# Kernel tuning notes

Measured on AMD Instinct MI355X. Metric: run time of the kernel, lower is better.

The kernel has to match this reference:

```python
import jax, jax.numpy as jnp
import numpy as np

H = 128       # hidden size
IN = 6        # input size
OUT = 1       # output size
B, T = 128, 2048


def setup_inputs() -> dict:
    key = jax.random.key(0)
    ks = jax.random.split(key, 16)
    s = 1.0 / np.sqrt(H)  # PyTorch LSTM init: U(-1/sqrt(H), 1/sqrt(H))
    u = lambda k, shape: jax.random.uniform(k, shape, jnp.float32, -s, s)
    inp = {"x": jax.random.normal(ks[0], (B, T, IN), jnp.float32)}
    in_sizes = [IN, H, H]
    for l in range(3):
        inp[f"W_ih{l}"] = u(ks[1 + 4 * l], (4 * H, in_sizes[l]))
        inp[f"W_hh{l}"] = u(ks[2 + 4 * l], (4 * H, H))
        inp[f"b_ih{l}"] = u(ks[3 + 4 * l], (4 * H,))
        inp[f"b_hh{l}"] = u(ks[4 + 4 * l], (4 * H,))
    inp["W_out"] = u(ks[13], (OUT, H))
    inp["b_out"] = u(ks[14], (OUT,))
    return inp


def _lstm_layer(x, W_ih, W_hh, b):
    # x: [B, T, D_in]; precompute input contribution once, scan the recurrence.
    xg = jnp.einsum("bti,gi->btg", x, W_ih) + b  # [B, T, 4H]
    h0 = jnp.zeros((x.shape[0], H), x.dtype)
    c0 = jnp.zeros((x.shape[0], H), x.dtype)

    def step(carry, xg_t):
        h, c = carry
        g = xg_t + h @ W_hh.T                     # [B, 4H]
        i, f, gg, o = jnp.split(g, 4, axis=-1)    # PyTorch gate order i,f,g,o
        i = jax.nn.sigmoid(i)
        f = jax.nn.sigmoid(f)
        gg = jnp.tanh(gg)
        o = jax.nn.sigmoid(o)
        c = f * c + i * gg
        h = o * jnp.tanh(c)
        return (h, c), h

    _, hs = jax.lax.scan(step, (h0, c0), jnp.swapaxes(xg, 0, 1))  # hs: [T, B, H]
    return jnp.swapaxes(hs, 0, 1)


def reference(x, W_ih0, W_hh0, b_ih0, b_hh0, W_ih1, W_hh1, b_ih1, b_hh1,
              W_ih2, W_hh2, b_ih2, b_hh2, W_out, b_out):
    # 3-layer LSTM (dropout inactive in eval mode) + linear head on last step.
    h = _lstm_layer(x, W_ih0, W_hh0, b_ih0 + b_hh0)
    h = _lstm_layer(h, W_ih1, W_hh1, b_ih1 + b_hh1)
    h = _lstm_layer(h, W_ih2, W_hh2, b_ih2 + b_hh2)
    return h[:, -1, :] @ W_out.T + b_out  # [B, 1]
```

## Files before the change

### kernel.cpp

```cpp
#include <hip/hip_runtime.h>

#define B_ 128
#define T_ 2048
#define H_ 128
#define IN_ 6
#define GRP_ 8
#define NGRP_ (T_ / GRP_)
#define CHUNK_ 32
#define NCHUNK_ (T_ / CHUNK_)
#define FLAG_STRIDE_ 64
#define HS_ 144
#define XGRING_ 3
#define XGSLOT_ (CHUNK_ * 8192)
#define NFLAGS_ 272

typedef _Float16 f16x8 __attribute__((ext_vector_type(8)));
typedef float    f32x4 __attribute__((ext_vector_type(4)));

__device__ __forceinline__ unsigned short f2h_u(float f) {
  union { _Float16 h; unsigned short u; } v; v.h = (_Float16)f; return v.u;
}
__device__ __forceinline__ unsigned int pack2(float a, float b) {
  return (unsigned int)f2h_u(a) | ((unsigned int)f2h_u(b) << 16);
}
__device__ __forceinline__ float sigf_(float x) {
  return __builtin_amdgcn_rcpf(1.0f + __expf(-x));
}
__device__ __forceinline__ float tanhf_(float x) {
  return 2.0f * __builtin_amdgcn_rcpf(1.0f + __expf(-2.0f * x)) - 1.0f;
}
__device__ __forceinline__ f16x8 load_w8(const float* __restrict__ p) {
  f16x8 r;
#pragma unroll
  for (int i = 0; i < 8; ++i) r[i] = (_Float16)p[i];
  return r;
}

__global__ void init_flags(unsigned int* flags) {
  flags[blockIdx.x * 256 + threadIdx.x] = 0u;
}

#define BARRIER_LGKM()                                              \
  do {                                                              \
    asm volatile("s_waitcnt lgkmcnt(0)" ::: "memory");              \
    __builtin_amdgcn_s_barrier();                                   \
    __builtin_amdgcn_sched_barrier(0);                              \
  } while (0)

#define PUBLISH_FENCE()                                             \
  do {                                                              \
    asm volatile("s_waitcnt vmcnt(0)" ::: "memory");                \
    __builtin_amdgcn_s_barrier();                                   \
  } while (0)

#define MFMA16(A, B, C) __builtin_amdgcn_mfma_f32_16x16x32_f16((A), (B), (C), 0, 0, 0)

__global__ __launch_bounds__(512, 2)
void lstm_pipe(const float* __restrict__ x,
               const float* __restrict__ Wih0, const float* __restrict__ Whh0,
               const float* __restrict__ bih0, const float* __restrict__ bhh0,
               const float* __restrict__ Wih1, const float* __restrict__ Whh1,
               const float* __restrict__ bih1, const float* __restrict__ bhh1,
               const float* __restrict__ Wih2, const float* __restrict__ Whh2,
               const float* __restrict__ bih2, const float* __restrict__ bhh2,
               unsigned short* __restrict__ region,
               float* __restrict__ xg,
               unsigned int* __restrict__ state_h,
               unsigned int* __restrict__ flags)
{
  const int bid  = blockIdx.x;
  const int tid  = threadIdx.x;
  const int lane = tid & 63;
  const int wv   = tid >> 6;
  const int n16  = lane & 15;
  const int quad = lane >> 4;

  __shared__ unsigned short smem[32 * 16 * HS_];
  __shared__ int s_have;

#define WAITP(ptr_, need_, have_)                                   \
  do {                                                              \
    if ((have_) < (need_)) {                                        \
      if (tid == 0) {                                               \
        int v = (int)__hip_atomic_load(ptr_, __ATOMIC_RELAXED,      \
                                       __HIP_MEMORY_SCOPE_AGENT);   \
        while (v < (need_)) {                                       \
          __builtin_amdgcn_s_sleep(2);                              \
          v = (int)__hip_atomic_load(ptr_, __ATOMIC_RELAXED,        \
                                     __HIP_MEMORY_SCOPE_AGENT);     \
        }                                                           \
        (void)__hip_atomic_load(ptr_, __ATOMIC_ACQUIRE,             \
                                __HIP_MEMORY_SCOPE_AGENT);          \
        s_have = v;                                                 \
      }                                                             \
      __syncthreads();                                              \
      (have_) = s_have;                                             \
    }                                                               \
  } while (0)

  if (bid >= 96) {
    const int gi = bid - 96;
    const int gl = 1 + (gi >> 3);
    const int bg = gi & 7;
    const int b8 = n16 & 7;
    const float* Wih = (gl == 1) ? Wih1 : Wih2;
    const float* bih = (gl == 1) ? bih1 : bih2;
    const float* bhh = (gl == 1) ? bhh1 : bhh2;
    float* xgo = xg + (size_t)((gl - 1) * 8 + bg) * (XGRING_ * (size_t)XGSLOT_);
    unsigned int* fhp[4]; unsigned int* fcp[4];
#pragma unroll
    for (int q = 0; q < 4; ++q) {
      fhp[q] = &flags[((gl - 1) * 32 + 4 * bg + q) * FLAG_STRIDE_];
      fcp[q] = &flags[(144 + (gl - 1) * 64 + 4 * bg + q) * FLAG_STRIDE_];
    }
    unsigned int* fx_out = &flags[(128 + (gl - 1) * 8 + bg) * FLAG_STRIDE_];

    f16x8 wih[4][4];
#pragma unroll
    for (int j = 0; j < 4; ++j)
#pragma unroll
      for (int kc = 0; kc < 4; ++kc)
        wih[j][kc] = load_w8(Wih + (size_t)(j * 128 + 16 * wv + n16) * H_ + kc * 32 + quad * 8);
    f32x4 bias4[4];
#pragma unroll
    for (int j = 0; j < 4; ++j)
#pragma unroll
      for (int r = 0; r < 4; ++r) {
        int row = j * 128 + 16 * wv + quad * 4 + r;
        bias4[j][r] = bih[row] + bhh[row];
      }

    int haveh0 = 0, haveh1 = 0, haveh2 = 0, haveh3 = 0;
    int havec0 = 0, havec1 = 0, havec2 = 0, havec3 = 0;
    const int tt = tid >> 4, bb = tid & 15;
    const int swk = bb & 7;
    for (int k = 0; k < NCHUNK_; ++k) {
      WAITP(fhp[0], k + 1, haveh0);
      WAITP(fhp[1], k + 1, haveh1);
      WAITP(fhp[2], k + 1, haveh2);
      WAITP(fhp[3], k + 1, haveh3);
      if (k >= XGRING_) {
        WAITP(fcp[0], k - (XGRING_ - 1), havec0);
        WAITP(fcp[1], k - (XGRING_ - 1), havec1);
        WAITP(fcp[2], k - (XGRING_ - 1), havec2);
        WAITP(fcp[3], k - (XGRING_ - 1), havec3);
      }
      {
        const uint4* gp = (const uint4*)(region +
            ((size_t)(bg * 16 + bb) * T_ + (size_t)(CHUNK_ * k + tt)) * H_);
        uint4* lp = (uint4*)&smem[(tt * 16 + bb) * HS_];
#pragma unroll
        for (int i = 0; i < 16; ++i) lp[i ^ swk] = gp[i];
      }
      __syncthreads();
      const int slot = k % XGRING_;
      for (int t = 0; t < CHUNK_; ++t) {
        f16x8 hi4[4];
#pragma unroll
        for (int kc = 0; kc < 4; ++kc)
          hi4[kc] = *(const f16x8*)&smem[(t * 16 + n16) * HS_ +
                                         ((kc * 32 + quad * 8) ^ (b8 << 3))];
        float* xp = xgo + (size_t)(slot * CHUNK_ + t) * 8192 + quad * 64 + n16 * 4;
#pragma unroll
        for (int j = 0; j < 4; ++j) {
          f32x4 a = bias4[j];
#pragma unroll
          for (int kc = 0; kc < 4; ++kc)
            a = MFMA16(wih[j][kc], hi4[kc], a);
          *(f32x4*)(xp + (size_t)(8 * j + wv) * 256) = a;
        }
      }
      __syncthreads();
      if (tid == 0)
        __hip_atomic_store(fx_out, (unsigned int)(k + 1),
                           __ATOMIC_RELEASE, __HIP_MEMORY_SCOPE_AGENT);
    }
    return;
  }

  const int layer = bid >> 5;
  const int sl    = bid & 31;
  const int bcol  = n16 & 3;
  const int rr    = n16 >> 2;
  const int batch = sl * 4 + bcol;
  const float* Whh = (layer == 0) ? Whh0 : ((layer == 1) ? Whh1 : Whh2);

  unsigned short* hstate = smem;
  unsigned short* xb = smem + 2 * 4 * HS_;

  f16x8 whh[4][4];
#pragma unroll
  for (int j = 0; j < 4; ++j)
#pragma unroll
    for (int kc = 0; kc < 4; ++kc)
      whh[j][kc] = load_w8(Whh + (size_t)(j * 128 + 16 * wv + n16) * H_ + kc * 32 + quad * 8);

  for (int i = tid; i < (2 * 4 * HS_) / 2; i += 512) ((unsigned int*)smem)[i] = 0u;

  float cc_ = 0.f;
  unsigned short dh16[GRP_];
  const bool r2 = (rr & 2) != 0, r1 = (rr & 1) != 0;
  const int hcol = 16 * wv + 4 * quad + rr;
  const int wswz = (((hcol >> 3) ^ bcol) << 3) | (hcol & 7);
  unsigned int* fh_out = (layer < 2) ? &flags[(layer * 32 + sl) * FLAG_STRIDE_] : nullptr;

#define SEL3(a_) (r1 ? (r2 ? (a_)[3] : (a_)[1]) : (r2 ? (a_)[2] : (a_)[0]))

  if (layer == 0) {
    f32x4 bias4[4];
#pragma unroll
    for (int j = 0; j < 4; ++j)
#pragma unroll
      for (int r = 0; r < 4; ++r) {
        int row = j * 128 + 16 * wv + quad * 4 + r;
        bias4[j][r] = bih0[row] + bhh0[row];
      }
    f16x8 wx[4];
#pragma unroll
    for (int j = 0; j < 4; ++j)
#pragma unroll
      for (int i = 0; i < 8; ++i) wx[j][i] = (_Float16)0.f;
    if (quad == 0) {
#pragma unroll
      for (int j = 0; j < 4; ++j) {
        const float* p = Wih0 + (size_t)(j * 128 + 16 * wv + n16) * IN_;
#pragma unroll
        for (int i = 0; i < IN_; ++i) wx[j][i] = (_Float16)p[i];
      }
    }
    const int sn_x = tid & 3, st_x = tid >> 2;
    float xraw[6];
    __syncthreads();
    if (tid < 32) {
      const float* xp = x + ((size_t)(sl * 4 + sn_x) * T_ + st_x) * IN_;
#pragma unroll
      for (int i = 0; i < IN_; ++i) xraw[i] = xp[i];
      uint4 xr4;
      xr4.x = pack2(xraw[0], xraw[1]); xr4.y = pack2(xraw[2], xraw[3]);
      xr4.z = pack2(xraw[4], xraw[5]); xr4.w = 0u;
      *(uint4*)&xb[(st_x * 4 + sn_x) * 8] = xr4;
    }
    __syncthreads();

    for (int g = 0; g < NGRP_; ++g) {
      if (tid < 32 && g + 1 < NGRP_) {
        const float* xp = x + ((size_t)(sl * 4 + sn_x) * T_ + (8 * (g + 1) + st_x)) * IN_;
#pragma unroll
        for (int i = 0; i < IN_; ++i) xraw[i] = xp[i];
      }
#pragma unroll
      for (int s = 0; s < GRP_; ++s) {
        const int rp = s & 1, wp = rp ^ 1;
        f16x8 hs[4];
#pragma unroll
        for (int kc = 0; kc < 4; ++kc)
          hs[kc] = *(const f16x8*)&hstate[(rp * 4 + bcol) * HS_ +
                                          ((kc * 32 + quad * 8) ^ (bcol << 3))];
        f16x8 xi;
#pragma unroll
        for (int i = 0; i < 8; ++i) xi[i] = (_Float16)0.f;
        if (quad == 0) xi = *(const f16x8*)&xb[(s * 4 + bcol) * 8];
        f32x4 a0 = MFMA16(wx[0], xi, bias4[0]);
        f32x4 a1 = MFMA16(wx[1], xi, bias4[1]);
#pragma unroll
        for (int kc = 0; kc < 4; ++kc) {
          a0 = MFMA16(whh[0][kc], hs[kc], a0);
          a1 = MFMA16(whh[1][kc], hs[kc], a1);
        }
        float gi = SEL3(a0), gf = SEL3(a1);
        float ei = __expf(-gi), ef = __expf(-gf);
        f32x4 a2 = MFMA16(wx[2], xi, bias4[2]);
        f32x4 a3 = MFMA16(wx[3], xi, bias4[3]);
#pragma unroll
        for (int kc = 0; kc < 4; ++kc) {
          a2 = MFMA16(whh[2][kc], hs[kc], a2);
          a3 = MFMA16(whh[3][kc], hs[kc], a3);
        }
        float gg = SEL3(a2), go = SEL3(a3);
        float i_ = __builtin_amdgcn_rcpf(1.0f + ei);
        float f_ = __builtin_amdgcn_rcpf(1.0f + ef);
        float t_ = tanhf_(gg), o_ = sigf_(go);
        cc_ = f_ * cc_ + i_ * t_;
        float h_ = o_ * tanhf_(cc_);
        unsigned short uh = f2h_u(h_);
        dh16[s] = uh;
        hstate[(wp * 4 + bcol) * HS_ + wswz] = uh;
        BARRIER_LGKM();
      }
#pragma unroll
      for (int s = 0; s < GRP_; ++s)
        region[((size_t)batch * T_ + (8 * g + s)) * H_ + hcol] = dh16[s];
      if (tid < 32 && g + 1 < NGRP_) {
        uint4 xr4;
        xr4.x = pack2(xraw[0], xraw[1]); xr4.y = pack2(xraw[2], xraw[3]);
        xr4.z = pack2(xraw[4], xraw[5]); xr4.w = 0u;
        *(uint4*)&xb[(st_x * 4 + sn_x) * 8] = xr4;
      }
      BARRIER_LGKM();
      if ((g & 3) == 3) {
        PUBLISH_FENCE();
        if (tid == 0)
          __hip_atomic_store(fh_out, (unsigned int)((g >> 2) + 1),
                             __ATOMIC_RELEASE, __HIP_MEMORY_SCOPE_AGENT);
      }
    }
  } else {
    const int bg = sl >> 2;
    const float* xgi = xg + (size_t)((layer - 1) * 8 + bg) * (XGRING_ * (size_t)XGSLOT_);
    const int lane_off = quad * 64 + ((sl & 3) * 4 + bcol) * 4 + wv * 256;
    f32x4 xr[2][4];
    auto load_xg = [&](const float* cb, int tin, int buf) {
      const float* p = cb + (size_t)tin * 8192 + lane_off;
      xr[buf][0] = *(const f32x4*)(p);
      xr[buf][1] = *(const f32x4*)(p + 2048);
      xr[buf][2] = *(const f32x4*)(p + 4096);
      xr[buf][3] = *(const f32x4*)(p + 6144);
    };
    unsigned int* fx_in  = &flags[(128 + (layer - 1) * 8 + bg) * FLAG_STRIDE_];
    unsigned int* fc_out = &flags[(144 + (layer - 1) * 64 + sl) * FLAG_STRIDE_];
    int have_x = 0;
    const float* cbase = xgi;
    __syncthreads();

    for (int g = 0; g < NGRP_; ++g) {
      if ((g & 3) == 0) {
        int c = g >> 2;
        WAITP(fx_in, c + 1, have_x);
        cbase = xgi + (size_t)((c % XGRING_) * CHUNK_) * 8192;
        load_xg(cbase, 0, 0);
        load_xg(cbase, 1, 1);
      }
#pragma unroll
      for (int s = 0; s < GRP_; ++s) {
        const int t = 8 * g + s;
        const int rp = s & 1, wp = rp ^ 1;
        f16x8 hs[4];
#pragma unroll
        for (int kc = 0; kc < 4; ++kc)
          hs[kc] = *(const f16x8*)&hstate[(rp * 4 + bcol) * HS_ +
                                          ((kc * 32 + quad * 8) ^ (bcol << 3))];
        f32x4 a0 = xr[s & 1][0];
        f32x4 a1 = xr[s & 1][1];
#pragma unroll
        for (int kc = 0; kc < 4; ++kc) {
          a0 = MFMA16(whh[0][kc], hs[kc], a0);
          a1 = MFMA16(whh[1][kc], hs[kc], a1);
        }
        float gi = SEL3(a0), gf = SEL3(a1);
        float ei = __expf(-gi), ef = __expf(-gf);
        f32x4 a2 = xr[s & 1][2];
        f32x4 a3 = xr[s & 1][3];
#pragma unroll
        for (int kc = 0; kc < 4; ++kc) {
          a2 = MFMA16(whh[2][kc], hs[kc], a2);
          a3 = MFMA16(whh[3][kc], hs[kc], a3);
        }
        if (!(((g & 3) == 3) && s >= 6)) load_xg(cbase, (t + 2) & 31, s & 1);
        float gg = SEL3(a2), go = SEL3(a3);
        float i_ = __builtin_amdgcn_rcpf(1.0f + ei);
        float f_ = __builtin_amdgcn_rcpf(1.0f + ef);
        float t_ = tanhf_(gg), o_ = sigf_(go);
        cc_ = f_ * cc_ + i_ * t_;
        float h_ = o_ * tanhf_(cc_);
        unsigned short uh = f2h_u(h_);
        dh16[s] = uh;
        hstate[(wp * 4 + bcol) * HS_ + wswz] = uh;
        BARRIER_LGKM();
      }
      if (layer == 1) {
#pragma unroll
        for (int s = 0; s < GRP_; ++s)
          region[((size_t)batch * T_ + (8 * g + s)) * H_ + hcol] = dh16[s];
      }
      if ((g & 3) == 3) {
        PUBLISH_FENCE();
        if (tid == 0) {
          unsigned int cdone = (unsigned int)((g >> 2) + 1);
          if (layer == 1)
            __hip_atomic_store(fh_out, cdone, __ATOMIC_RELEASE, __HIP_MEMORY_SCOPE_AGENT);
          __hip_atomic_store(fc_out, cdone, __ATOMIC_RELEASE, __HIP_MEMORY_SCOPE_AGENT);
        }
      }
    }
    if (layer == 2)
      ((unsigned short*)state_h)[(size_t)batch * 128 + hcol] = dh16[GRP_ - 1];
  }
#undef WAITP
#undef SEL3
}

__global__ void head_kernel(const unsigned int* __restrict__ state_h,
                            const float* __restrict__ Wout,
                            const float* __restrict__ bout,
                            float* __restrict__ out)
{
  int b = threadIdx.x;
  float s = bout[0];
  for (int j = 0; j < 64; ++j) {
    unsigned int p = state_h[b * 64 + j];
    union { unsigned short u; _Float16 h; } lo, hi;
    lo.u = (unsigned short)(p & 0xffffu);
    hi.u = (unsigned short)(p >> 16);
    s += (float)lo.h * Wout[2 * j] + (float)hi.h * Wout[2 * j + 1];
  }
  out[b] = s;
}

extern "C" void kernel_launch(void* const* d_in, const int* in_sizes, int n_in,
                              void* d_out, int out_size, void* d_ws, size_t ws_size,
                              hipStream_t stream)
{
  const float* x = (const float*)d_in[0];
  const float* Wih[3] = {(const float*)d_in[1], (const float*)d_in[5], (const float*)d_in[9]};
  const float* Whh[3] = {(const float*)d_in[2], (const float*)d_in[6], (const float*)d_in[10]};
  const float* bih[3] = {(const float*)d_in[3], (const float*)d_in[7], (const float*)d_in[11]};
  const float* bhh[3] = {(const float*)d_in[4], (const float*)d_in[8], (const float*)d_in[12]};
  const float* Wout = (const float*)d_in[13];
  const float* bout = (const float*)d_in[14];
  float* out = (float*)d_out;

  char* ws = (char*)d_ws;
  size_t off = 0;
  unsigned short* region = (unsigned short*)(ws + off); off += (size_t)B_ * T_ * H_ * 2;
  float* xg = (float*)(ws + off);                       off += (size_t)16 * XGRING_ * XGSLOT_ * 4;
  unsigned int* state_h  = (unsigned int*)(ws + off);   off += (size_t)B_ * 64 * 4;
  off = (off + 255) & ~(size_t)255;
  unsigned int* flags    = (unsigned int*)(ws + off);   off += NFLAGS_ * FLAG_STRIDE_ * 4;

  init_flags<<<68, 256, 0, stream>>>(flags);
  lstm_pipe<<<112, 512, 0, stream>>>(x,
      Wih[0], Whh[0], bih[0], bhh[0],
      Wih[1], Whh[1], bih[1], bhh[1],
      Wih[2], Whh[2], bih[2], bhh[2],
      region, xg, state_h, flags);
  head_kernel<<<1, 128, 0, stream>>>(state_h, Wout, bout, out);
}
```

Baseline: 1.542 ms.

## Interleave two batch halves per recurrent block and offload layer-0 input projection

```diff
diff --git a/kernel.cpp b/kernel.cpp
--- a/kernel.cpp
+++ b/kernel.cpp
@@ -4,15 +4,13 @@
 #define T_ 2048
 #define H_ 128
 #define IN_ 6
-#define GRP_ 8
-#define NGRP_ (T_ / GRP_)
 #define CHUNK_ 32
-#define NCHUNK_ (T_ / CHUNK_)
+#define NCHUNK_ 64
 #define FLAG_STRIDE_ 64
 #define HS_ 144
-#define XGRING_ 3
 #define XGSLOT_ (CHUNK_ * 8192)
-#define NFLAGS_ 272
+#define XGRING_ 2
+#define NFLAGS_ 184
 
 typedef _Float16 f16x8 __attribute__((ext_vector_type(8)));
 typedef float    f32x4 __attribute__((ext_vector_type(4)));
@@ -100,20 +98,84 @@
 
   if (bid >= 96) {
     const int gi = bid - 96;
-    const int gl = 1 + (gi >> 3);
+    const int gl = gi >> 3;
     const int bg = gi & 7;
+    float* xgo = xg + (size_t)(gl * 8 + bg) * (XGRING_ * (size_t)XGSLOT_);
+    unsigned int* fx_out = &flags[(64 + gl * 8 + bg) * FLAG_STRIDE_];
+    unsigned int* fcp[4];
+#pragma unroll
+    for (int q = 0; q < 4; ++q)
+      fcp[q] = &flags[(88 + gl * 32 + 4 * bg + q) * FLAG_STRIDE_];
+
+    if (gl == 0) {
+      f16x8 wih[4];
+#pragma unroll
+      for (int j = 0; j < 4; ++j)
+#pragma unroll
+        for (int i = 0; i < 8; ++i) wih[j][i] = (_Float16)0.f;
+      if (quad == 0) {
+#pragma unroll
+        for (int j = 0; j < 4; ++j) {
+          const float* p = Wih0 + (size_t)(j * 128 + 16 * wv + n16) * IN_;
+#pragma unroll
+          for (int i = 0; i < IN_; ++i) wih[j][i] = (_Float16)p[i];
+        }
+      }
+      f32x4 bias4[4];
+#pragma unroll
+      for (int j = 0; j < 4; ++j)
+#pragma unroll
+        for (int r = 0; r < 4; ++r) {
+          int row = j * 128 + 16 * wv + quad * 4 + r;
+          bias4[j][r] = bih0[row] + bhh0[row];
+        }
+      unsigned short* xbp = smem;
+      const int tt = tid >> 4, bb = tid & 15;
+      int hc0 = 0, hc1 = 0, hc2 = 0, hc3 = 0;
+      for (int k = 0; k < NCHUNK_; ++k) {
+        if (k >= XGRING_) {
+          WAITP(fcp[0], k - (XGRING_ - 1), hc0);
+          WAITP(fcp[1], k - (XGRING_ - 1), hc1);
+          WAITP(fcp[2], k - (XGRING_ - 1), hc2);
+          WAITP(fcp[3], k - (XGRING_ - 1), hc3);
+        }
+        {
+          const float* xp = x + ((size_t)(bg * 16 + bb) * T_ + (size_t)(CHUNK_ * k + tt)) * IN_;
+          uint4 v;
+          v.x = pack2(xp[0], xp[1]); v.y = pack2(xp[2], xp[3]);
+          v.z = pack2(xp[4], xp[5]); v.w = 0u;
+          *(uint4*)&xbp[(tt * 16 + bb) * 8] = v;
+        }
+        __syncthreads();
+        const int slot = k & 1;
+        for (int t = 0; t < CHUNK_; ++t) {
+          f16x8 xi;
+#pragma unroll
+          for (int i = 0; i < 8; ++i) xi[i] = (_Float16)0.f;
+          if (quad == 0) xi = *(const f16x8*)&xbp[(t * 16 + n16) * 8];
+          float* xp = xgo + (size_t)(slot * CHUNK_ + t) * 8192 + quad * 64 + n16 * 4;
+#pragma unroll
+          for (int j = 0; j < 4; ++j) {
+            f32x4 a = MFMA16(wih[j], xi, bias4[j]);
+            *(f32x4*)(xp + (size_t)(8 * j + wv) * 256) = a;
+          }
+        }
+        __syncthreads();
+        if (tid == 0)
+          __hip_atomic_store(fx_out, (unsigned int)(k + 1),
+                             __ATOMIC_RELEASE, __HIP_MEMORY_SCOPE_AGENT);
+      }
+      return;
+    }
+
     const int b8 = n16 & 7;
     const float* Wih = (gl == 1) ? Wih1 : Wih2;
     const float* bih = (gl == 1) ? bih1 : bih2;
     const float* bhh = (gl == 1) ? bhh1 : bhh2;
-    float* xgo = xg + (size_t)((gl - 1) * 8 + bg) * (XGRING_ * (size_t)XGSLOT_);
-    unsigned int* fhp[4]; unsigned int* fcp[4];
-#pragma unroll
-    for (int q = 0; q < 4; ++q) {
+    unsigned int* fhp[4];
+#pragma unroll
+    for (int q = 0; q < 4; ++q)
       fhp[q] = &flags[((gl - 1) * 32 + 4 * bg + q) * FLAG_STRIDE_];
-      fcp[q] = &flags[(144 + (gl - 1) * 64 + 4 * bg + q) * FLAG_STRIDE_];
-    }
-    unsigned int* fx_out = &flags[(128 + (gl - 1) * 8 + bg) * FLAG_STRIDE_];
 
     f16x8 wih[4][4];
 #pragma unroll
@@ -130,20 +192,20 @@
         bias4[j][r] = bih[row] + bhh[row];
       }
 
-    int haveh0 = 0, haveh1 = 0, haveh2 = 0, haveh3 = 0;
-    int havec0 = 0, havec1 = 0, havec2 = 0, havec3 = 0;
+    int hh0 = 0, hh1 = 0, hh2 = 0, hh3 = 0;
+    int hc0 = 0, hc1 = 0, hc2 = 0, hc3 = 0;
     const int tt = tid >> 4, bb = tid & 15;
     const int swk = bb & 7;
     for (int k = 0; k < NCHUNK_; ++k) {
-      WAITP(fhp[0], k + 1, haveh0);
-      WAITP(fhp[1], k + 1, haveh1);
-      WAITP(fhp[2], k + 1, haveh2);
-      WAITP(fhp[3], k + 1, haveh3);
+      WAITP(fhp[0], k + 1, hh0);
+      WAITP(fhp[1], k + 1, hh1);
+      WAITP(fhp[2], k + 1, hh2);
+      WAITP(fhp[3], k + 1, hh3);
       if (k >= XGRING_) {
-        WAITP(fcp[0], k - (XGRING_ - 1), havec0);
-        WAITP(fcp[1], k - (XGRING_ - 1), havec1);
-        WAITP(fcp[2], k - (XGRING_ - 1), havec2);
-        WAITP(fcp[3], k - (XGRING_ - 1), havec3);
+        WAITP(fcp[0], k - (XGRING_ - 1), hc0);
+        WAITP(fcp[1], k - (XGRING_ - 1), hc1);
+        WAITP(fcp[2], k - (XGRING_ - 1), hc2);
+        WAITP(fcp[3], k - (XGRING_ - 1), hc3);
       }
       {
         const uint4* gp = (const uint4*)(region +
@@ -153,7 +215,7 @@
         for (int i = 0; i < 16; ++i) lp[i ^ swk] = gp[i];
       }
       __syncthreads();
-      const int slot = k % XGRING_;
+      const int slot = k & 1;
       for (int t = 0; t < CHUNK_; ++t) {
         f16x8 hi4[4];
 #pragma unroll
@@ -180,13 +242,16 @@
 
   const int layer = bid >> 5;
   const int sl    = bid & 31;
-  const int bcol  = n16 & 3;
-  const int rr    = n16 >> 2;
-  const int batch = sl * 4 + bcol;
+  const int bcol1 = n16 & 1;
+  const int rr    = (n16 >> 1) & 3;
+  const bool actv = (n16 < 8);
+  const bool r1 = (rr & 1) != 0, r2 = (rr & 2) != 0;
+  const int hidx = 16 * wv + 4 * quad + rr;
+  const int bA = sl * 4 + bcol1;
+  const int bB = sl * 4 + 2 + bcol1;
   const float* Whh = (layer == 0) ? Whh0 : ((layer == 1) ? Whh1 : Whh2);
 
   unsigned short* hstate = smem;
-  unsigned short* xb = smem + 2 * 4 * HS_;
 
   f16x8 whh[4][4];
 #pragma unroll
@@ -195,198 +260,146 @@
     for (int kc = 0; kc < 4; ++kc)
       whh[j][kc] = load_w8(Whh + (size_t)(j * 128 + 16 * wv + n16) * H_ + kc * 32 + quad * 8);
 
-  for (int i = tid; i < (2 * 4 * HS_) / 2; i += 512) ((unsigned int*)smem)[i] = 0u;
-
-  float cc_ = 0.f;
-  unsigned short dh16[GRP_];
-  const bool r2 = (rr & 2) != 0, r1 = (rr & 1) != 0;
-  const int hcol = 16 * wv + 4 * quad + rr;
-  const int wswz = (((hcol >> 3) ^ bcol) << 3) | (hcol & 7);
+  for (int i = tid; i < (4 * HS_) / 2; i += 512) ((unsigned int*)smem)[i] = 0u;
+
+  const float* xgi = xg + (size_t)(layer * 8 + (sl >> 2)) * (XGRING_ * (size_t)XGSLOT_);
+  const int laneA = wv * 256 + quad * 64 + ((sl & 3) * 4 + 0 + bcol1) * 4;
+  const int laneB = wv * 256 + quad * 64 + ((sl & 3) * 4 + 2 + bcol1) * 4;
+  unsigned int* fx_in  = &flags[(64 + layer * 8 + (sl >> 2)) * FLAG_STRIDE_];
+  unsigned int* fc_out = &flags[(88 + layer * 32 + sl) * FLAG_STRIDE_];
   unsigned int* fh_out = (layer < 2) ? &flags[(layer * 32 + sl) * FLAG_STRIDE_] : nullptr;
+  unsigned short* regA = region + (size_t)bA * T_ * H_ + hidx;
+  unsigned short* regB = region + (size_t)bB * T_ * H_ + hidx;
+
+  float cA = 0.f, cB = 0.f;
+  f32x4 accP0 = {0,0,0,0}, accP1 = {0,0,0,0}, accP2 = {0,0,0,0}, accP3 = {0,0,0,0};
+  f32x4 xrA[4], xrB[4];
+  unsigned short dhA[8], dhB[8];
+  int slotA = 0, slotB = 0;
+  int have_x = 0;
 
 #define SEL3(a_) (r1 ? (r2 ? (a_)[3] : (a_)[1]) : (r2 ? (a_)[2] : (a_)[0]))
-
-  if (layer == 0) {
-    f32x4 bias4[4];
-#pragma unroll
-    for (int j = 0; j < 4; ++j)
-#pragma unroll
-      for (int r = 0; r < 4; ++r) {
-        int row = j * 128 + 16 * wv + quad * 4 + r;
-        bias4[j][r] = bih0[row] + bhh0[row];
-      }
-    f16x8 wx[4];
-#pragma unroll
-    for (int j = 0; j < 4; ++j)
-#pragma unroll
-      for (int i = 0; i < 8; ++i) wx[j][i] = (_Float16)0.f;
-    if (quad == 0) {
-#pragma unroll
-      for (int j = 0; j < 4; ++j) {
-        const float* p = Wih0 + (size_t)(j * 128 + 16 * wv + n16) * IN_;
-#pragma unroll
-        for (int i = 0; i < IN_; ++i) wx[j][i] = (_Float16)p[i];
-      }
-    }
-    const int sn_x = tid & 3, st_x = tid >> 2;
-    float xraw[6];
-    __syncthreads();
-    if (tid < 32) {
-      const float* xp = x + ((size_t)(sl * 4 + sn_x) * T_ + st_x) * IN_;
-#pragma unroll
-      for (int i = 0; i < IN_; ++i) xraw[i] = xp[i];
-      uint4 xr4;
-      xr4.x = pack2(xraw[0], xraw[1]); xr4.y = pack2(xraw[2], xraw[3]);
-      xr4.z = pack2(xraw[4], xraw[5]); xr4.w = 0u;
-      *(uint4*)&xb[(st_x * 4 + sn_x) * 8] = xr4;
-    }
-    __syncthreads();
-
-    for (int g = 0; g < NGRP_; ++g) {
-      if (tid < 32 && g + 1 < NGRP_) {
-        const float* xp = x + ((size_t)(sl * 4 + sn_x) * T_ + (8 * (g + 1) + st_x)) * IN_;
-#pragma unroll
-        for (int i = 0; i < IN_; ++i) xraw[i] = xp[i];
-      }
-#pragma unroll
-      for (int s = 0; s < GRP_; ++s) {
-        const int rp = s & 1, wp = rp ^ 1;
-        f16x8 hs[4];
-#pragma unroll
-        for (int kc = 0; kc < 4; ++kc)
-          hs[kc] = *(const f16x8*)&hstate[(rp * 4 + bcol) * HS_ +
-                                          ((kc * 32 + quad * 8) ^ (bcol << 3))];
-        f16x8 xi;
-#pragma unroll
-        for (int i = 0; i < 8; ++i) xi[i] = (_Float16)0.f;
-        if (quad == 0) xi = *(const f16x8*)&xb[(s * 4 + bcol) * 8];
-        f32x4 a0 = MFMA16(wx[0], xi, bias4[0]);
-        f32x4 a1 = MFMA16(wx[1], xi, bias4[1]);
-#pragma unroll
-        for (int kc = 0; kc < 4; ++kc) {
-          a0 = MFMA16(whh[0][kc], hs[kc], a0);
-          a1 = MFMA16(whh[1][kc], hs[kc], a1);
-        }
-        float gi = SEL3(a0), gf = SEL3(a1);
-        float ei = __expf(-gi), ef = __expf(-gf);
-        f32x4 a2 = MFMA16(wx[2], xi, bias4[2]);
-        f32x4 a3 = MFMA16(wx[3], xi, bias4[3]);
-#pragma unroll
-        for (int kc = 0; kc < 4; ++kc) {
-          a2 = MFMA16(whh[2][kc], hs[kc], a2);
-          a3 = MFMA16(whh[3][kc], hs[kc], a3);
-        }
-        float gg = SEL3(a2), go = SEL3(a3);
-        float i_ = __builtin_amdgcn_rcpf(1.0f + ei);
-        float f_ = __builtin_amdgcn_rcpf(1.0f + ef);
-        float t_ = tanhf_(gg), o_ = sigf_(go);
-        cc_ = f_ * cc_ + i_ * t_;
-        float h_ = o_ * tanhf_(cc_);
-        unsigned short uh = f2h_u(h_);
-        dh16[s] = uh;
-        hstate[(wp * 4 + bcol) * HS_ + wswz] = uh;
-        BARRIER_LGKM();
-      }
-#pragma unroll
-      for (int s = 0; s < GRP_; ++s)
-        region[((size_t)batch * T_ + (8 * g + s)) * H_ + hcol] = dh16[s];
-      if (tid < 32 && g + 1 < NGRP_) {
-        uint4 xr4;
-        xr4.x = pack2(xraw[0], xraw[1]); xr4.y = pack2(xraw[2], xraw[3]);
-        xr4.z = pack2(xraw[4], xraw[5]); xr4.w = 0u;
-        *(uint4*)&xb[(st_x * 4 + sn_x) * 8] = xr4;
-      }
+#define ACT1(aP0_, aP1_, aP2_, aP3_, c_, uh_)                        \
+  do {                                                               \
+    float vi = SEL3(aP0_), vf = SEL3(aP1_);                          \
+    float vg = SEL3(aP2_), vo = SEL3(aP3_);                          \
+    float i_ = sigf_(vi), f_ = sigf_(vf);                            \
+    float t_ = tanhf_(vg), o_ = sigf_(vo);                           \
+    (c_) = f_ * (c_) + i_ * t_;                                      \
+    (uh_) = f2h_u(o_ * tanhf_(c_));                                  \
+  } while (0)
+
+  WAITP(fx_in, 1, have_x);
+#pragma unroll
+  for (int j = 0; j < 4; ++j) {
+    xrA[j] = *(const f32x4*)(xgi + (size_t)j * 2048 + laneA);
+    xrB[j] = *(const f32x4*)(xgi + (size_t)j * 2048 + laneB);
+  }
+  __syncthreads();
+
+  for (int gg = 0; gg < 256; ++gg) {
+#pragma unroll
+    for (int s = 0; s < 8; ++s) {
+      const int p = 8 * gg + s;
       BARRIER_LGKM();
-      if ((g & 3) == 3) {
-        PUBLISH_FENCE();
-        if (tid == 0)
-          __hip_atomic_store(fh_out, (unsigned int)((g >> 2) + 1),
-                             __ATOMIC_RELEASE, __HIP_MEMORY_SCOPE_AGENT);
-      }
-    }
-  } else {
-    const int bg = sl >> 2;
-    const float* xgi = xg + (size_t)((layer - 1) * 8 + bg) * (XGRING_ * (size_t)XGSLOT_);
-    const int lane_off = quad * 64 + ((sl & 3) * 4 + bcol) * 4 + wv * 256;
-    f32x4 xr[2][4];
-    auto load_xg = [&](const float* cb, int tin, int buf) {
-      const float* p = cb + (size_t)tin * 8192 + lane_off;
-      xr[buf][0] = *(const f32x4*)(p);
-      xr[buf][1] = *(const f32x4*)(p + 2048);
-      xr[buf][2] = *(const f32x4*)(p + 4096);
-      xr[buf][3] = *(const f32x4*)(p + 6144);
-    };
-    unsigned int* fx_in  = &flags[(128 + (layer - 1) * 8 + bg) * FLAG_STRIDE_];
-    unsigned int* fc_out = &flags[(144 + (layer - 1) * 64 + sl) * FLAG_STRIDE_];
-    int have_x = 0;
-    const float* cbase = xgi;
-    __syncthreads();
-
-    for (int g = 0; g < NGRP_; ++g) {
-      if ((g & 3) == 0) {
-        int c = g >> 2;
-        WAITP(fx_in, c + 1, have_x);
-        cbase = xgi + (size_t)((c % XGRING_) * CHUNK_) * 8192;
-        load_xg(cbase, 0, 0);
-        load_xg(cbase, 1, 1);
-      }
-#pragma unroll
-      for (int s = 0; s < GRP_; ++s) {
-        const int t = 8 * g + s;
-        const int rp = s & 1, wp = rp ^ 1;
-        f16x8 hs[4];
-#pragma unroll
-        for (int kc = 0; kc < 4; ++kc)
-          hs[kc] = *(const f16x8*)&hstate[(rp * 4 + bcol) * HS_ +
-                                          ((kc * 32 + quad * 8) ^ (bcol << 3))];
-        f32x4 a0 = xr[s & 1][0];
-        f32x4 a1 = xr[s & 1][1];
-#pragma unroll
-        for (int kc = 0; kc < 4; ++kc) {
-          a0 = MFMA16(whh[0][kc], hs[kc], a0);
-          a1 = MFMA16(whh[1][kc], hs[kc], a1);
-        }
-        float gi = SEL3(a0), gf = SEL3(a1);
-        float ei = __expf(-gi), ef = __expf(-gf);
-        f32x4 a2 = xr[s & 1][2];
-        f32x4 a3 = xr[s & 1][3];
-#pragma unroll
-        for (int kc = 0; kc < 4; ++kc) {
-          a2 = MFMA16(whh[2][kc], hs[kc], a2);
-          a3 = MFMA16(whh[3][kc], hs[kc], a3);
-        }
-        if (!(((g & 3) == 3) && s >= 6)) load_xg(cbase, (t + 2) & 31, s & 1);
-        float gg = SEL3(a2), go = SEL3(a3);
-        float i_ = __builtin_amdgcn_rcpf(1.0f + ei);
-        float f_ = __builtin_amdgcn_rcpf(1.0f + ef);
-        float t_ = tanhf_(gg), o_ = sigf_(go);
-        cc_ = f_ * cc_ + i_ * t_;
-        float h_ = o_ * tanhf_(cc_);
-        unsigned short uh = f2h_u(h_);
-        dh16[s] = uh;
-        hstate[(wp * 4 + bcol) * HS_ + wswz] = uh;
-        BARRIER_LGKM();
-      }
-      if (layer == 1) {
-#pragma unroll
-        for (int s = 0; s < GRP_; ++s)
-          region[((size_t)batch * T_ + (8 * g + s)) * H_ + hcol] = dh16[s];
-      }
-      if ((g & 3) == 3) {
+      f16x8 hA0 = *(const f16x8*)&hstate[(0 * 2 + bcol1) * HS_ + 0 * 32 + quad * 8];
+      f16x8 hA1 = *(const f16x8*)&hstate[(0 * 2 + bcol1) * HS_ + 1 * 32 + quad * 8];
+      f16x8 hA2 = *(const f16x8*)&hstate[(0 * 2 + bcol1) * HS_ + 2 * 32 + quad * 8];
+      f16x8 hA3 = *(const f16x8*)&hstate[(0 * 2 + bcol1) * HS_ + 3 * 32 + quad * 8];
+      if (gg > 0 || s > 0) {
+        unsigned short uh;
+        ACT1(accP0, accP1, accP2, accP3, cB, uh);
+        if (actv) hstate[(1 * 2 + bcol1) * HS_ + hidx] = uh;
+        dhB[(s == 0) ? 7 : (s - 1)] = uh;
+        if (s == 0 && layer < 2 && actv) {
+#pragma unroll
+          for (int k = 0; k < 8; ++k) regB[(size_t)(p - 8 + k) * H_] = dhB[k];
+        }
+      }
+      f32x4 aN0 = MFMA16(whh[0][0], hA0, xrA[0]);
+      f32x4 aN1 = MFMA16(whh[1][0], hA0, xrA[1]);
+      f32x4 aN2 = MFMA16(whh[2][0], hA0, xrA[2]);
+      f32x4 aN3 = MFMA16(whh[3][0], hA0, xrA[3]);
+      aN0 = MFMA16(whh[0][1], hA1, aN0); aN1 = MFMA16(whh[1][1], hA1, aN1);
+      aN2 = MFMA16(whh[2][1], hA1, aN2); aN3 = MFMA16(whh[3][1], hA1, aN3);
+      aN0 = MFMA16(whh[0][2], hA2, aN0); aN1 = MFMA16(whh[1][2], hA2, aN1);
+      aN2 = MFMA16(whh[2][2], hA2, aN2); aN3 = MFMA16(whh[3][2], hA2, aN3);
+      aN0 = MFMA16(whh[0][3], hA3, aN0); aN1 = MFMA16(whh[1][3], hA3, aN1);
+      aN2 = MFMA16(whh[2][3], hA3, aN2); aN3 = MFMA16(whh[3][3], hA3, aN3);
+      if (s == 7 && (gg & 3) == 3 && gg != 255)
+        WAITP(fx_in, ((gg + 1) >> 2) + 1, have_x);
+      if (p < 2047) {
+        const int tn = p + 1;
+        if ((tn & 31) == 0) slotA ^= 1;
+        const float* pA = xgi + (size_t)slotA * XGSLOT_ + (size_t)(tn & 31) * 8192 + laneA;
+#pragma unroll
+        for (int j = 0; j < 4; ++j) xrA[j] = *(const f32x4*)(pA + (size_t)j * 2048);
+      }
+      if (s == 0 && (gg & 3) == 0 && gg > 0) {
         PUBLISH_FENCE();
         if (tid == 0) {
-          unsigned int cdone = (unsigned int)((g >> 2) + 1);
-          if (layer == 1)
+          unsigned int cdone = (unsigned int)(gg >> 2);
+          if (layer < 2)
             __hip_atomic_store(fh_out, cdone, __ATOMIC_RELEASE, __HIP_MEMORY_SCOPE_AGENT);
           __hip_atomic_store(fc_out, cdone, __ATOMIC_RELEASE, __HIP_MEMORY_SCOPE_AGENT);
         }
       }
+      BARRIER_LGKM();
+      f16x8 hB0 = *(const f16x8*)&hstate[(1 * 2 + bcol1) * HS_ + 0 * 32 + quad * 8];
+      f16x8 hB1 = *(const f16x8*)&hstate[(1 * 2 + bcol1) * HS_ + 1 * 32 + quad * 8];
+      f16x8 hB2 = *(const f16x8*)&hstate[(1 * 2 + bcol1) * HS_ + 2 * 32 + quad * 8];
+      f16x8 hB3 = *(const f16x8*)&hstate[(1 * 2 + bcol1) * HS_ + 3 * 32 + quad * 8];
+      {
+        unsigned short uh;
+        ACT1(aN0, aN1, aN2, aN3, cA, uh);
+        if (actv) hstate[(0 * 2 + bcol1) * HS_ + hidx] = uh;
+        dhA[s] = uh;
+        if (s == 7 && layer < 2 && actv) {
+#pragma unroll
+          for (int k = 0; k < 8; ++k) regA[(size_t)(p - 7 + k) * H_] = dhA[k];
+        }
+      }
+      accP0 = MFMA16(whh[0][0], hB0, xrB[0]);
+      accP1 = MFMA16(whh[1][0], hB0, xrB[1]);
+      accP2 = MFMA16(whh[2][0], hB0, xrB[2]);
+      accP3 = MFMA16(whh[3][0], hB0, xrB[3]);
+      accP0 = MFMA16(whh[0][1], hB1, accP0); accP1 = MFMA16(whh[1][1], hB1, accP1);
+      accP2 = MFMA16(whh[2][1], hB1, accP2); accP3 = MFMA16(whh[3][1], hB1, accP3);
+      accP0 = MFMA16(whh[0][2], hB2, accP0); accP1 = MFMA16(whh[1][2], hB2, accP1);
+      accP2 = MFMA16(whh[2][2], hB2, accP2); accP3 = MFMA16(whh[3][2], hB2, accP3);
+      accP0 = MFMA16(whh[0][3], hB3, accP0); accP1 = MFMA16(whh[1][3], hB3, accP1);
+      accP2 = MFMA16(whh[2][3], hB3, accP2); accP3 = MFMA16(whh[3][3], hB3, accP3);
+      if (p < 2047) {
+        const int tn = p + 1;
+        if ((tn & 31) == 0) slotB ^= 1;
+        const float* pB = xgi + (size_t)slotB * XGSLOT_ + (size_t)(tn & 31) * 8192 + laneB;
+#pragma unroll
+        for (int j = 0; j < 4; ++j) xrB[j] = *(const f32x4*)(pB + (size_t)j * 2048);
+      }
     }
-    if (layer == 2)
-      ((unsigned short*)state_h)[(size_t)batch * 128 + hcol] = dh16[GRP_ - 1];
-  }
+  }
+  {
+    unsigned short uh;
+    ACT1(accP0, accP1, accP2, accP3, cB, uh);
+    dhB[7] = uh;
+    if (layer < 2 && actv) {
+#pragma unroll
+      for (int k = 0; k < 8; ++k) regB[(size_t)(2040 + k) * H_] = dhB[k];
+    }
+    if (layer == 2 && actv) {
+      ((unsigned short*)state_h)[(size_t)bA * 128 + hidx] = dhA[7];
+      ((unsigned short*)state_h)[(size_t)bB * 128 + hidx] = dhB[7];
+    }
+  }
+  PUBLISH_FENCE();
+  if (tid == 0) {
+    if (layer < 2)
+      __hip_atomic_store(fh_out, 64u, __ATOMIC_RELEASE, __HIP_MEMORY_SCOPE_AGENT);
+    __hip_atomic_store(fc_out, 64u, __ATOMIC_RELEASE, __HIP_MEMORY_SCOPE_AGENT);
+  }
+#undef SEL3
+#undef ACT1
 #undef WAITP
-#undef SEL3
 }
 
 __global__ void head_kernel(const unsigned int* __restrict__ state_h,
@@ -422,13 +435,13 @@
   char* ws = (char*)d_ws;
   size_t off = 0;
   unsigned short* region = (unsigned short*)(ws + off); off += (size_t)B_ * T_ * H_ * 2;
-  float* xg = (float*)(ws + off);                       off += (size_t)16 * XGRING_ * XGSLOT_ * 4;
+  float* xg = (float*)(ws + off);                       off += (size_t)24 * XGRING_ * XGSLOT_ * 4;
   unsigned int* state_h  = (unsigned int*)(ws + off);   off += (size_t)B_ * 64 * 4;
   off = (off + 255) & ~(size_t)255;
   unsigned int* flags    = (unsigned int*)(ws + off);   off += NFLAGS_ * FLAG_STRIDE_ * 4;
 
-  init_flags<<<68, 256, 0, stream>>>(flags);
-  lstm_pipe<<<112, 512, 0, stream>>>(x,
+  init_flags<<<46, 256, 0, stream>>>(flags);
+  lstm_pipe<<<120, 512, 0, stream>>>(x,
       Wih[0], Whh[0], bih[0], bhh[0],
       Wih[1], Whh[1], bih[1], bhh[1],
       Wih[2], Whh[2], bih[2], bhh[2],
```

After: 2.402 ms. 1.56x slower.
